# Optimization experiments

Hardware: AMD Instinct MI355X
Metric: run time of the kernel (lower is better)

The kernel has to match this reference:

```python
import jax, jax.numpy as jnp
import numpy as np

N = 50000      # num_nodes
E = 400000     # num_edges
ND = 128       # node_dim (== hidden_dim of GraphNetwork)
HID = 128      # per-head hidden dim in GAT layer
HEADS = 4      # GAT default num_heads
L = 3          # num_layers


def setup_inputs() -> dict:
    key = jax.random.key(0)
    ks = jax.random.split(key, 12)
    s = lambda k, shape, fan: (jax.random.normal(k, shape, jnp.float32) / np.sqrt(fan)).astype(jnp.float32)
    return dict(
        node_features=jax.random.normal(ks[0], (N, ND), jnp.float32),
        edge_index=jax.random.randint(ks[1], (2, E), 0, N, dtype=jnp.int32),
        enc_w1=s(ks[2], (ND, HID), ND), enc_b1=jnp.zeros((HID,), jnp.float32),
        enc_w2=s(ks[3], (HID, HID), HID), enc_b2=jnp.zeros((HID,), jnp.float32),
        gat_W=s(ks[4], (L, HID, HEADS * HID), HID),
        gat_a_src=s(ks[5], (L, HEADS, HID), HID),
        gat_a_dst=s(ks[6], (L, HEADS, HID), HID),
        gat_out_w=s(ks[7], (L, HEADS * HID, HID), HEADS * HID),
        gat_out_b=jnp.zeros((L, HID), jnp.float32),
        out_w1=s(ks[8], (HID, HID), HID), out_b1=jnp.zeros((HID,), jnp.float32),
        out_w2=s(ks[9], (HID, HID), HID), out_b2=jnp.zeros((HID,), jnp.float32),
    )


def _gat_layer(x, row, col, W, a_src, a_dst, ow, ob):
    """One GraphAttentionLayer (eval mode: dropout disabled)."""
    n = x.shape[0]
    h = (x @ W).reshape(n, HEADS, HID)                       # [N,H,D]
    # per-node attention logits (equivalent to (h[row]*a_src).sum(-1) gathered)
    s_src = jnp.einsum('nhd,hd->nh', h, a_src)               # [N,H]
    s_dst = jnp.einsum('nhd,hd->nh', h, a_dst)               # [N,H]
    e = s_src[row] + s_dst[col]                              # [E,H]
    e = jnp.where(e > 0, e, 0.2 * e)                         # LeakyReLU(0.2)
    e_exp = jnp.exp(e)                                       # matches torch: raw exp, no max-shift
    e_sum = jax.ops.segment_sum(e_exp, col, num_segments=n)  # [N,H]
    alpha = e_exp / (e_sum[col] + 1e-8)                      # [E,H]
    msg = h[row] * alpha[:, :, None]                         # [E,H,D]
    out = jax.ops.segment_sum(msg, col, num_segments=n)      # [N,H,D]
    out = out.reshape(n, HEADS * HID) @ ow + ob              # out_proj
    return x + out                                           # residual


def reference(node_features, edge_index, enc_w1, enc_b1, enc_w2, enc_b2,
              gat_W, gat_a_src, gat_a_dst, gat_out_w, gat_out_b,
              out_w1, out_b1, out_w2, out_b2):
    row, col = edge_index[0], edge_index[1]
    # node encoder: Linear-ReLU-Linear
    h = jax.nn.relu(node_features @ enc_w1 + enc_b1) @ enc_w2 + enc_b2
    for i in range(L):
        h = _gat_layer(h, row, col, gat_W[i], gat_a_src[i], gat_a_dst[i],
                       gat_out_w[i], gat_out_b[i])
    # output MLP: Linear-ReLU-Linear
    h = jax.nn.relu(h @ out_w1 + out_b1) @ out_w2 + out_b2
    # batch is None, global_pooling='mean'
    graph_embedding = h.mean(axis=0, keepdims=True)          # [1,HID]
    return h, graph_embedding
```

## Files before the change

### kernel.cpp

```cpp
#include <hip/hip_runtime.h>
#include <math.h>

typedef unsigned short ushort_t;
typedef __attribute__((ext_vector_type(8))) unsigned short ushortx8;
typedef __attribute__((ext_vector_type(4))) unsigned short ushortx4;
typedef __attribute__((ext_vector_type(4))) float floatx4;
typedef __attribute__((ext_vector_type(8))) short frag8;

__device__ __forceinline__ float bf2f(ushort_t u){
  union {unsigned int i; float f;} v; v.i = ((unsigned int)u)<<16; return v.f;
}
__device__ __forceinline__ ushort_t f2bf(float f){
  union {float f; unsigned int i;} v; v.f = f;
  unsigned int x = v.i;
  unsigned int r = x + 0x7fffu + ((x>>16)&1u);
  return (ushort_t)(r>>16);
}

__device__ __forceinline__ void gload16(const void* g, void* l){
  __builtin_amdgcn_global_load_lds(
      (const __attribute__((address_space(1))) unsigned int*)g,
      (__attribute__((address_space(3))) unsigned int*)l, 16, 0, 0);
}

__global__ __launch_bounds__(256) void k_count(const int* __restrict__ col, int* __restrict__ cnt, int E){
  int e = blockIdx.x*256 + threadIdx.x;
  if (e < E) atomicAdd(&cnt[col[e]], 1);
}

__global__ __launch_bounds__(256) void k_scan1(const int* __restrict__ cnt, int* __restrict__ offs,
                                               int* __restrict__ partials, int n){
  __shared__ int buf[256];
  int tid = threadIdx.x;
  int gid = blockIdx.x*256 + tid;
  int v = (gid < n) ? cnt[gid] : 0;
  buf[tid] = v; __syncthreads();
  #pragma unroll
  for (int off=1; off<256; off<<=1){
    int t = (tid >= off) ? buf[tid-off] : 0;
    __syncthreads();
    buf[tid] += t;
    __syncthreads();
  }
  if (gid < n) offs[gid] = buf[tid] - v;
  if (tid == 255) partials[blockIdx.x] = buf[255];
}

__global__ __launch_bounds__(256) void k_scan2(int* __restrict__ partials, int nb){
  __shared__ int buf[256];
  int tid = threadIdx.x;
  int v = (tid < nb) ? partials[tid] : 0;
  buf[tid] = v; __syncthreads();
  #pragma unroll
  for (int off=1; off<256; off<<=1){
    int t = (tid >= off) ? buf[tid-off] : 0;
    __syncthreads();
    buf[tid] += t;
    __syncthreads();
  }
  partials[tid] = buf[tid] - v;
}

__global__ __launch_bounds__(256) void k_scan3(int* __restrict__ offs, const int* __restrict__ partials,
                                               int n, int E){
  int gid = blockIdx.x*256 + threadIdx.x;
  if (gid < n) offs[gid] += partials[blockIdx.x];
  if (blockIdx.x == 0 && threadIdx.x == 0) offs[n] = E;
}

__global__ __launch_bounds__(256) void k_fill(const int* __restrict__ row, const int* __restrict__ col,
                                              const int* __restrict__ offs, int* __restrict__ fill,
                                              int* __restrict__ rowS, int E){
  int e = blockIdx.x*256 + threadIdx.x;
  if (e >= E) return;
  int c = col[e];
  int pos = offs[c] + atomicAdd(&fill[c], 1);
  rowS[pos] = row[e];
}

template<int K, int NC, int CNT>
__global__ __launch_bounds__(256) void k_convT_b(const float* __restrict__ src, ushort_t* __restrict__ dst){
  int idx = blockIdx.x*256 + threadIdx.x;
  if (idx >= CNT*K*NC) return;
  int l = idx / (K*NC);
  int rem = idx - l*(K*NC);
  int k = rem / NC, n = rem - k*NC;
  dst[(size_t)l*K*NC + (size_t)n*K + k] = f2bf(src[idx]);
}

__global__ __launch_bounds__(256) void k_convT4(const float* __restrict__ s0, const float* __restrict__ s1,
                                                const float* __restrict__ s2, const float* __restrict__ s3,
                                                ushort_t* __restrict__ d0, ushort_t* __restrict__ d1,
                                                ushort_t* __restrict__ d2, ushort_t* __restrict__ d3){
  int idx = blockIdx.x*256 + threadIdx.x;
  if (idx >= 4*16384) return;
  int which = idx >> 14;
  int rem = idx & 16383;
  int k = rem >> 7, n = rem & 127;
  const float* s = which==0 ? s0 : which==1 ? s1 : which==2 ? s2 : s3;
  ushort_t*    d = which==0 ? d0 : which==1 ? d1 : which==2 ? d2 : d3;
  d[n*128 + k] = f2bf(s[rem]);
}


__device__ __forceinline__ void stage_tile64(const ushort_t* src, int ld, int row0, int M, int kc,
                                             ushort_t* lds, int tid){
  int wid = tid>>6, lane = tid&63;
  #pragma unroll
  for (int i=0;i<4;i++){
    int chunk = wid*256 + i*64 + lane;
    int r = chunk>>3, c8 = chunk&7;
    int gr = row0 + r; if (gr >= M) gr = M-1;
    gload16(src + (size_t)gr*ld + kc + c8*8, (char*)lds + (size_t)chunk*16);
  }
}
__device__ __forceinline__ void stage_w128(const ushort_t* src, ushort_t* lds, int tid){
  #pragma unroll
  for (int i=0;i<8;i++){
    int chunk = tid + 256*i;
    gload16(src + (size_t)chunk*8, (char*)lds + (size_t)chunk*16);
  }
}

template<int SA,int SB,int NKS>
__device__ __forceinline__ void ldsgemm(const ushort_t* LA, const ushort_t* LB,
                                        floatx4 (&acc)[4][4], int wr,int wc,int lm,int lk){
  #pragma unroll
  for (int ks=0; ks<NKS; ks++){
    frag8 a[4], b[4];
    #pragma unroll
    for (int mi=0;mi<4;mi++) a[mi] = *(const frag8*)&LA[(wr+mi*16+lm)*SA + ks*32 + lk];
    #pragma unroll
    for (int ni=0;ni<4;ni++) b[ni] = *(const frag8*)&LB[(wc+ni*16+lm)*SB + ks*32 + lk];
    #pragma unroll
    for (int mi=0;mi<4;mi++)
      #pragma unroll
      for (int ni=0;ni<4;ni++)
        acc[mi][ni] = __builtin_amdgcn_mfma_f32_16x16x32_bf16(b[ni], a[mi], acc[mi][ni], 0, 0, 0);
  }
}

__device__ __forceinline__ void zero_acc(floatx4 (&acc)[4][4]){
  #pragma unroll
  for (int i=0;i<4;i++)
    #pragma unroll
    for (int j=0;j<4;j++) acc[i][j] = floatx4{0.f,0.f,0.f,0.f};
}

__device__ __forceinline__ void sdst_block(const floatx4 (&acc)[4][4],
    const float* avec_s, const float* avec_d, float* s_src, float* s_dst, float* sred,
    int head, int bm, int M, int tid, int wid, int lane, int wr, int wc, int lm, int lr4){
  floatx4 avs[4], avd[4];
  #pragma unroll
  for (int ni=0;ni<4;ni++){
    avs[ni] = *(const floatx4*)&avec_s[head*128 + wc + ni*16 + lr4];
    avd[ni] = *(const floatx4*)&avec_d[head*128 + wc + ni*16 + lr4];
  }
  #pragma unroll
  for (int mi=0;mi<4;mi++){
    float vs = 0.f, vd = 0.f;
    #pragma unroll
    for (int ni=0;ni<4;ni++)
      #pragma unroll
      for (int r=0;r<4;r++){
        float v = acc[mi][ni][r];
        vs += v * avs[ni][r];
        vd += v * avd[ni][r];
      }
    vs += __shfl_xor(vs, 16); vs += __shfl_xor(vs, 32);
    vd += __shfl_xor(vd, 16); vd += __shfl_xor(vd, 32);
    if (lane < 16){
      int rl = wr + mi*16 + lm;
      sred[0*256 + (wid&1)*128 + rl] = vs;
      sred[1*256 + (wid&1)*128 + rl] = vd;
    }
  }
  __syncthreads();
  int sd = tid >> 7, rl = tid & 127;
  float v = sred[sd*256 + rl] + sred[sd*256 + 128 + rl];
  int rowg = bm + rl;
  if (rowg < M) (sd ? s_dst : s_src)[(size_t)rowg*4 + head] = v;
}

__device__ __forceinline__ void wgemm_heads(const ushort_t* LA_xb, ushort_t* LB,
    const ushort_t* WT, const float* avs, const float* avd,
    ushort_t* h, float* s_src, float* s_dst, float* sred,
    int bm, int M, int tid, int wid, int lane, int wr, int wc, int lm, int lk, int lr4){
  for (int hb=0; hb<4; hb++){
    __syncthreads();
    stage_w128(WT + (size_t)hb*16384, LB, tid);
    __syncthreads();
    floatx4 acc[4][4]; zero_acc(acc);
    ldsgemm<128,128,4>(LA_xb, LB, acc, wr, wc, lm, lk);
    #pragma unroll
    for (int mi=0;mi<4;mi++){
      int rowg = bm + wr + mi*16 + lm;
      if (rowg < M){
        #pragma unroll
        for (int ni=0;ni<4;ni++){
          int coll = wc + ni*16 + lr4;
          ushortx4 o;
          #pragma unroll
          for (int r=0;r<4;r++) o[r] = f2bf(acc[mi][ni][r]);
          *(ushortx4*)&h[(size_t)rowg*512 + hb*128 + coll] = o;
        }
      }
    }
    sdst_block(acc, avs, avd, s_src, s_dst, sred, hb, bm, M, tid, wid, lane, wr, wc, lm, lr4);
  }
}

__global__ __launch_bounds__(256) void k_enc(
    const float* __restrict__ nodef,
    const ushort_t* __restrict__ e1T, const float* __restrict__ eb1,
    const ushort_t* __restrict__ e2T, const float* __restrict__ eb2,
    const ushort_t* __restrict__ WT, const float* __restrict__ avs, const float* __restrict__ avd,
    float* __restrict__ x, ushort_t* __restrict__ h,
    float* __restrict__ s_src, float* __restrict__ s_dst, int M)
{
  __shared__ ushort_t LA[128*128];
  __shared__ ushort_t LB[128*128];
  __shared__ float sred[512];
  const int tid = threadIdx.x, wid = tid>>6, lane = tid&63;
  const int bm = blockIdx.x*128;
  const int wr = (wid>>1)*64, wc = (wid&1)*64, lm = lane&15, lk = (lane>>4)*8, lr4 = (lane>>4)*4;

  #pragma unroll
  for (int i=0;i<8;i++){
    int chunk = tid + 256*i;
    int r = chunk>>4, c8 = chunk&15;
    int gr = bm + r; if (gr >= M) gr = M-1;
    floatx4 lo = *(const floatx4*)(nodef + (size_t)gr*128 + c8*8);
    floatx4 hi = *(const floatx4*)(nodef + (size_t)gr*128 + c8*8 + 4);
    ushortx8 v;
    #pragma unroll
    for (int j=0;j<4;j++){ v[j] = f2bf(lo[j]); v[j+4] = f2bf(hi[j]); }
    *(ushortx8*)&LA[r*128 + c8*8] = v;
  }
  stage_w128(e1T, LB, tid);
  __syncthreads();

  floatx4 acc[4][4]; zero_acc(acc);
  ldsgemm<128,128,4>(LA, LB, acc, wr, wc, lm, lk);
  __syncthreads();
  #pragma unroll
  for (int mi=0;mi<4;mi++){
    int rl = wr + mi*16 + lm;
    #pragma unroll
    for (int ni=0;ni<4;ni++){
      int coll = wc + ni*16 + lr4;
      floatx4 b4 = *(const floatx4*)&eb1[coll];
      ushortx4 o;
      #pragma unroll
      for (int r=0;r<4;r++){
        float v = acc[mi][ni][r] + b4[r];
        v = v > 0.f ? v : 0.f;
        o[r] = f2bf(v);
      }
      *(ushortx4*)&LA[rl*128 + coll] = o;
    }
  }
  stage_w128(e2T, LB, tid);
  __syncthreads();

  zero_acc(acc);
  ldsgemm<128,128,4>(LA, LB, acc, wr, wc, lm, lk);
  __syncthreads();
  #pragma unroll
  for (int mi=0;mi<4;mi++){
    int rl = wr + mi*16 + lm;
    int rowg = bm + rl;
    #pragma unroll
    for (int ni=0;ni<4;ni++){
      int coll = wc + ni*16 + lr4;
      floatx4 b4 = *(const floatx4*)&eb2[coll];
      floatx4 v;
      #pragma unroll
      for (int r=0;r<4;r++) v[r] = acc[mi][ni][r] + b4[r];
      if (rowg < M) *(floatx4*)&x[(size_t)rowg*128 + coll] = v;
      ushortx4 o;
      #pragma unroll
      for (int r=0;r<4;r++) o[r] = f2bf(v[r]);
      *(ushortx4*)&LA[rl*128 + coll] = o;
    }
  }

  wgemm_heads(LA, LB, WT, avs, avd, h, s_src, s_dst, sred,
              bm, M, tid, wid, lane, wr, wc, lm, lk, lr4);
}

__global__ __launch_bounds__(256) void k_mid(
    const ushort_t* __restrict__ msg, const ushort_t* __restrict__ OT, const float* __restrict__ ob,
    const ushort_t* __restrict__ WT, const float* __restrict__ avs, const float* __restrict__ avd,
    float* __restrict__ x, ushort_t* __restrict__ h,
    float* __restrict__ s_src, float* __restrict__ s_dst, int M)
{
  __shared__ ushort_t LA[128*128];
  __shared__ ushort_t LB[128*128];
  __shared__ float sred[512];
  const int tid = threadIdx.x, wid = tid>>6, lane = tid&63;
  const int bm = blockIdx.x*128;
  const int wr = (wid>>1)*64, wc = (wid&1)*64, lm = lane&15, lk = (lane>>4)*8, lr4 = (lane>>4)*4;

  floatx4 acc[4][4]; zero_acc(acc);
  for (int kc = 0; kc < 512; kc += 64){
    stage_tile64(msg, 512, bm, M, kc, LA, tid);
    stage_tile64(OT,  512, 0, 128, kc, LB, tid);
    __syncthreads();
    ldsgemm<64,64,2>(LA, LB, acc, wr, wc, lm, lk);
    __syncthreads();
  }
  #pragma unroll
  for (int mi=0;mi<4;mi++){
    int rl = wr + mi*16 + lm;
    int rowg = bm + rl;
    #pragma unroll
    for (int ni=0;ni<4;ni++){
      int coll = wc + ni*16 + lr4;
      floatx4 b4 = *(const floatx4*)&ob[coll];
      floatx4 v;
      #pragma unroll
      for (int r=0;r<4;r++) v[r] = acc[mi][ni][r] + b4[r];
      if (rowg < M){
        floatx4 xo = *(const floatx4*)&x[(size_t)rowg*128 + coll];
        #pragma unroll
        for (int r=0;r<4;r++) v[r] += xo[r];
        *(floatx4*)&x[(size_t)rowg*128 + coll] = v;
      }
      ushortx4 o;
      #pragma unroll
      for (int r=0;r<4;r++) o[r] = f2bf(v[r]);
      *(ushortx4*)&LA[rl*128 + coll] = o;
    }
  }

  wgemm_heads(LA, LB, WT, avs, avd, h, s_src, s_dst, sred,
              bm, M, tid, wid, lane, wr, wc, lm, lk, lr4);
}

__global__ __launch_bounds__(256) void k_tail(
    const ushort_t* __restrict__ msg, const ushort_t* __restrict__ OT, const float* __restrict__ ob,
    const ushort_t* __restrict__ m1T, const float* __restrict__ mb1,
    const ushort_t* __restrict__ m2T, const float* __restrict__ mb2,
    const float* __restrict__ x, float* __restrict__ out, float* __restrict__ cpart, int M)
{
  __shared__ ushort_t LA[128*128];
  __shared__ ushort_t LB[128*128];
  __shared__ float sredc[256];
  const int tid = threadIdx.x, wid = tid>>6, lane = tid&63;
  const int bm = blockIdx.x*128;
  const int wr = (wid>>1)*64, wc = (wid&1)*64, lm = lane&15, lk = (lane>>4)*8, lr4 = (lane>>4)*4;

  floatx4 acc[4][4]; zero_acc(acc);
  for (int kc = 0; kc < 512; kc += 64){
    stage_tile64(msg, 512, bm, M, kc, LA, tid);
    stage_tile64(OT,  512, 0, 128, kc, LB, tid);
    __syncthreads();
    ldsgemm<64,64,2>(LA, LB, acc, wr, wc, lm, lk);
    __syncthreads();
  }
  #pragma unroll
  for (int mi=0;mi<4;mi++){
    int rl = wr + mi*16 + lm;
    int rowg = bm + rl;
    #pragma unroll
    for (int ni=0;ni<4;ni++){
      int coll = wc + ni*16 + lr4;
      floatx4 b4 = *(const floatx4*)&ob[coll];
      floatx4 v;
      #pragma unroll
      for (int r=0;r<4;r++) v[r] = acc[mi][ni][r] + b4[r];
      if (rowg < M){
        floatx4 xo = *(const floatx4*)&x[(size_t)rowg*128 + coll];
        #pragma unroll
        for (int r=0;r<4;r++) v[r] += xo[r];
      }
      ushortx4 o;
      #pragma unroll
      for (int r=0;r<4;r++) o[r] = f2bf(v[r]);
      *(ushortx4*)&LA[rl*128 + coll] = o;
    }
  }
  stage_w128(m1T, LB, tid);
  __syncthreads();

  zero_acc(acc);
  ldsgemm<128,128,4>(LA, LB, acc, wr, wc, lm, lk);
  __syncthreads();
  #pragma unroll
  for (int mi=0;mi<4;mi++){
    int rl = wr + mi*16 + lm;
    #pragma unroll
    for (int ni=0;ni<4;ni++){
      int coll = wc + ni*16 + lr4;
      floatx4 b4 = *(const floatx4*)&mb1[coll];
      ushortx4 o;
      #pragma unroll
      for (int r=0;r<4;r++){
        float v = acc[mi][ni][r] + b4[r];
        v = v > 0.f ? v : 0.f;
        o[r] = f2bf(v);
      }
      *(ushortx4*)&LA[rl*128 + coll] = o;
    }
  }
  stage_w128(m2T, LB, tid);
  __syncthreads();

  zero_acc(acc);
  ldsgemm<128,128,4>(LA, LB, acc, wr, wc, lm, lk);

  float csum[4][4];
  #pragma unroll
  for (int i=0;i<4;i++)
    #pragma unroll
    for (int r=0;r<4;r++) csum[i][r] = 0.f;
  #pragma unroll
  for (int mi=0;mi<4;mi++){
    int rowg = bm + wr + mi*16 + lm;
    #pragma unroll
    for (int ni=0;ni<4;ni++){
      int coll = wc + ni*16 + lr4;
      floatx4 b4 = *(const floatx4*)&mb2[coll];
      floatx4 v;
      #pragma unroll
      for (int r=0;r<4;r++) v[r] = acc[mi][ni][r] + b4[r];
      if (rowg < M){
        *(floatx4*)&out[(size_t)rowg*128 + coll] = v;
        #pragma unroll
        for (int r=0;r<4;r++) csum[ni][r] += v[r];
      }
    }
  }
  __syncthreads();
  #pragma unroll
  for (int ni=0;ni<4;ni++)
    #pragma unroll
    for (int r=0;r<4;r++){
      float cs = csum[ni][r];
      cs += __shfl_xor(cs, 1);
      cs += __shfl_xor(cs, 2);
      cs += __shfl_xor(cs, 4);
      cs += __shfl_xor(cs, 8);
      if (lm == 0) sredc[(wid>>1)*128 + wc + ni*16 + lr4 + r] = cs;
    }
  __syncthreads();
  if (tid < 128) cpart[(size_t)blockIdx.x*128 + tid] = sredc[tid] + sredc[128 + tid];
}

__global__ __launch_bounds__(256) void k_gather(const ushort_t* __restrict__ h,
    const float* __restrict__ s_src, const float* __restrict__ s_dst,
    const int* __restrict__ offs, const int* __restrict__ rowS,
    ushort_t* __restrict__ msg, int N)
{
  int wid = threadIdx.x >> 6, lane = threadIdx.x & 63;
  int n = blockIdx.x*4 + wid;
  if (n >= N) return;
  int beg = offs[n], end = offs[n+1];
  const int sub  = lane & 15;
  const int head = lane >> 4;
  const float sdv = s_dst[(size_t)n*4 + head];
  const int c0 = lane*8;

  float acc[8];
  #pragma unroll
  for (int k=0;k<8;k++) acc[k] = 0.f;
  float dsum = 0.f;

  for (int chunk = beg; chunk < end; chunk += 16){
    int m = end - chunk; if (m > 16) m = 16;
    int q = chunk + (sub < m ? sub : m-1);
    int r_p = rowS[q];
    float ss = s_src[(size_t)r_p*4 + head];
    float e = ss + sdv;
    e = e > 0.f ? e : 0.2f*e;
    float w = __expf(e);
    if (sub >= m) w = 0.f;
    dsum += w;

    int j = 0;
    for (; j+1 < m; j += 2){
      int r0 = __shfl(r_p, j);
      int r1 = __shfl(r_p, j+1);
      float w0 = __shfl(w, head*16 + j);
      float w1 = __shfl(w, head*16 + j+1);
      ushortx8 h0 = *(const ushortx8*)(h + (size_t)r0*512 + c0);
      ushortx8 h1 = *(const ushortx8*)(h + (size_t)r1*512 + c0);
      #pragma unroll
      for (int k=0;k<8;k++) acc[k] += w0 * bf2f(h0[k]);
      #pragma unroll
      for (int k=0;k<8;k++) acc[k] += w1 * bf2f(h1[k]);
    }
    if (j < m){
      int r0 = __shfl(r_p, j);
      float w0 = __shfl(w, head*16 + j);
      ushortx8 h0 = *(const ushortx8*)(h + (size_t)r0*512 + c0);
      #pragma unroll
      for (int k=0;k<8;k++) acc[k] += w0 * bf2f(h0[k]);
    }
  }

  float d = dsum;
  #pragma unroll
  for (int mask=1; mask<16; mask<<=1) d += __shfl_xor(d, mask);
  float invd = 1.0f / (d + 1e-8f);

  ushortx8 o;
  #pragma unroll
  for (int k=0;k<8;k++) o[k] = f2bf(acc[k]*invd);
  __builtin_nontemporal_store(o, (ushortx8*)(msg + (size_t)n*512 + c0));
}

__global__ __launch_bounds__(256) void k_csum2(const float* __restrict__ part, float* __restrict__ out,
                                               int nb, int N){
  __shared__ float buf[256];
  int c = threadIdx.x & 127, half = threadIdx.x >> 7;
  float s = 0.f;
  for (int b = half; b < nb; b += 2) s += part[(size_t)b*128 + c];
  buf[threadIdx.x] = s; __syncthreads();
  if (threadIdx.x < 128) out[c] = (buf[c] + buf[128 + c]) / (float)N;
}

extern "C" void kernel_launch(void* const* d_in, const int* in_sizes, int n_in,
                              void* d_out, int out_size, void* d_ws, size_t ws_size,
                              hipStream_t stream)
{
  const int N = in_sizes[0] / 128;
  const int E = in_sizes[1] / 2;

  const float* nodef  = (const float*)d_in[0];
  const int*   row    = (const int*)d_in[1];
  const int*   col    = row + E;
  const float* enc_w1 = (const float*)d_in[2];
  const float* enc_b1 = (const float*)d_in[3];
  const float* enc_w2 = (const float*)d_in[4];
  const float* enc_b2 = (const float*)d_in[5];
  const float* gat_W  = (const float*)d_in[6];
  const float* a_src  = (const float*)d_in[7];
  const float* a_dst  = (const float*)d_in[8];
  const float* out_w  = (const float*)d_in[9];
  const float* out_b  = (const float*)d_in[10];
  const float* w1     = (const float*)d_in[11];
  const float* b1     = (const float*)d_in[12];
  const float* w2     = (const float*)d_in[13];
  const float* b2     = (const float*)d_in[14];

  char* p = (char*)d_ws;
  auto alloc = [&](size_t bytes)->char*{
    char* r = p; p += (bytes + 255) & ~(size_t)255; return r;
  };
  float*    x     = (float*)   alloc((size_t)N*128*4);
  ushort_t* msg   = (ushort_t*)alloc((size_t)N*512*2);
  ushort_t* h     = (ushort_t*)alloc((size_t)N*512*2);
  float*    s_src = (float*)   alloc((size_t)N*4*4);
  float*    s_dst = (float*)   alloc((size_t)N*4*4);
  int*      offs  = (int*)     alloc(((size_t)N+1)*4);
  int*      rowS  = (int*)     alloc((size_t)E*4);
  int*      cnt   = (int*)     alloc((size_t)N*4);
  int*      fill  = (int*)     alloc((size_t)N*4);
  int*      parts = (int*)     alloc(1024);
  float*    cpart = (float*)   alloc((size_t)((N+127)/128)*128*4);
  ushort_t* wt_e1 = (ushort_t*)alloc(16384*2);
  ushort_t* wt_e2 = (ushort_t*)alloc(16384*2);
  ushort_t* wt_W  = (ushort_t*)alloc((size_t)3*65536*2);
  ushort_t* wt_o  = (ushort_t*)alloc((size_t)3*65536*2);
  ushort_t* wt_m1 = (ushort_t*)alloc(16384*2);
  ushort_t* wt_m2 = (ushort_t*)alloc(16384*2);

  hipMemsetAsync(cnt, 0, (size_t)N*4, stream);
  hipMemsetAsync(fill, 0, (size_t)N*4, stream);

  const int gE = (E + 255)/256;
  const int gN = (N + 255)/256;
  const int gW = (N + 3)/4;
  const int gy = (N + 127)/128;
  dim3 blk(256);

  k_count<<<gE, blk, 0, stream>>>(col, cnt, E);
  k_scan1<<<gN, blk, 0, stream>>>(cnt, offs, parts, N);
  k_scan2<<<1,  blk, 0, stream>>>(parts, gN);
  k_scan3<<<gN, blk, 0, stream>>>(offs, parts, N, E);
  k_fill <<<gE, blk, 0, stream>>>(row, col, offs, fill, rowS, E);

  k_convT4<<<(4*16384+255)/256, blk, 0, stream>>>(enc_w1, enc_w2, w1, w2, wt_e1, wt_e2, wt_m1, wt_m2);
  k_convT_b<128,512,3><<<(3*65536+255)/256, blk, 0, stream>>>(gat_W, wt_W);
  k_convT_b<512,128,3><<<(3*65536+255)/256, blk, 0, stream>>>(out_w, wt_o);

  k_enc<<<gy, blk, 0, stream>>>(nodef, wt_e1, enc_b1, wt_e2, enc_b2,
                                wt_W, a_src, a_dst, x, h, s_src, s_dst, N);

  for (int l = 0; l < 3; l++){
    k_gather<<<gW, blk, 0, stream>>>(h, s_src, s_dst, offs, rowS, msg, N);
    if (l < 2){
      k_mid<<<gy, blk, 0, stream>>>(msg, wt_o + (size_t)l*65536, out_b + (size_t)l*128,
                                    wt_W + (size_t)(l+1)*65536,
                                    a_src + (size_t)(l+1)*512, a_dst + (size_t)(l+1)*512,
                                    x, h, s_src, s_dst, N);
    } else {
      k_tail<<<gy, blk, 0, stream>>>(msg, wt_o + (size_t)2*65536, out_b + (size_t)2*128,
                                     wt_m1, b1, wt_m2, b2,
                                     x, (float*)d_out, cpart, N);
    }
  }
  k_csum2<<<1, blk, 0, stream>>>(cpart, (float*)d_out + (size_t)N*128, gy, N);
}
```

Measured before the change: 511.0 us.

## Double-buffer weight and activation LDS staging across all fused GEMM kernels

Replaces the single-buffered LDS staging (load tile, sync, compute, sync) with a two-slot ping-pong scheme. The next 64-wide K slice of weights and messages is issued via global_load_lds while the current slice feeds the MFMAs. Weight tiles are also prefetched during epilogues. The aim is to hide global-load latency behind compute. The cost is more complex buffer indexing and synchronisation, with the same LDS footprint.

```diff
diff --git a/kernel.cpp b/kernel.cpp
--- a/kernel.cpp
+++ b/kernel.cpp
@@ -114,13 +114,6 @@
     gload16(src + (size_t)gr*ld + kc + c8*8, (char*)lds + (size_t)chunk*16);
   }
 }
-__device__ __forceinline__ void stage_w128(const ushort_t* src, ushort_t* lds, int tid){
-  #pragma unroll
-  for (int i=0;i<8;i++){
-    int chunk = tid + 256*i;
-    gload16(src + (size_t)chunk*8, (char*)lds + (size_t)chunk*16);
-  }
-}
 
 template<int SA,int SB,int NKS>
 __device__ __forceinline__ void ldsgemm(const ushort_t* LA, const ushort_t* LB,
@@ -182,31 +175,39 @@
   if (rowg < M) (sd ? s_dst : s_src)[(size_t)rowg*4 + head] = v;
 }
 
-__device__ __forceinline__ void wgemm_heads(const ushort_t* LA_xb, ushort_t* LB,
-    const ushort_t* WT, const float* avs, const float* avd,
-    ushort_t* h, float* s_src, float* s_dst, float* sred,
+__device__ __forceinline__ void wgemm_heads_db(ushort_t* SM,
+    const ushort_t* __restrict__ WT, const float* avsv, const float* avdv,
+    ushort_t* __restrict__ h, float* __restrict__ s_src, float* __restrict__ s_dst, float* sred,
     int bm, int M, int tid, int wid, int lane, int wr, int wc, int lm, int lk, int lr4){
-  for (int hb=0; hb<4; hb++){
-    __syncthreads();
-    stage_w128(WT + (size_t)hb*16384, LB, tid);
-    __syncthreads();
-    floatx4 acc[4][4]; zero_acc(acc);
-    ldsgemm<128,128,4>(LA_xb, LB, acc, wr, wc, lm, lk);
-    #pragma unroll
-    for (int mi=0;mi<4;mi++){
-      int rowg = bm + wr + mi*16 + lm;
-      if (rowg < M){
-        #pragma unroll
-        for (int ni=0;ni<4;ni++){
-          int coll = wc + ni*16 + lr4;
-          ushortx4 o;
+  floatx4 acc[4][4];
+  #pragma unroll
+  for (int ht=0; ht<8; ht++){
+    const int cur = ht&1;
+    if (ht<7){
+      const int nhb = (ht+1)>>1, nkph = (ht+1)&1;
+      stage_tile64(WT + (size_t)nhb*16384, 128, 0, 128, nkph*64, SM + 16384 + (cur^1)*8192, tid);
+    }
+    if ((ht&1)==0) zero_acc(acc);
+    ldsgemm<128,64,2>(SM + (ht&1)*64, SM + 16384 + cur*8192, acc, wr, wc, lm, lk);
+    if (ht&1){
+      const int hb = ht>>1;
+      #pragma unroll
+      for (int mi=0;mi<4;mi++){
+        int rowg = bm + wr + mi*16 + lm;
+        if (rowg < M){
           #pragma unroll
-          for (int r=0;r<4;r++) o[r] = f2bf(acc[mi][ni][r]);
-          *(ushortx4*)&h[(size_t)rowg*512 + hb*128 + coll] = o;
+          for (int ni=0;ni<4;ni++){
+            int coll = wc + ni*16 + lr4;
+            ushortx4 o;
+            #pragma unroll
+            for (int r=0;r<4;r++) o[r] = f2bf(acc[mi][ni][r]);
+            *(ushortx4*)&h[(size_t)rowg*512 + hb*128 + coll] = o;
+          }
         }
       }
-    }
-    sdst_block(acc, avs, avd, s_src, s_dst, sred, hb, bm, M, tid, wid, lane, wr, wc, lm, lr4);
+      sdst_block(acc, avsv, avdv, s_src, s_dst, sred, hb, bm, M, tid, wid, lane, wr, wc, lm, lr4);
+    }
+    __syncthreads();
   }
 }
 
@@ -218,12 +219,13 @@
     float* __restrict__ x, ushort_t* __restrict__ h,
     float* __restrict__ s_src, float* __restrict__ s_dst, int M)
 {
-  __shared__ ushort_t LA[128*128];
-  __shared__ ushort_t LB[128*128];
+  __shared__ ushort_t SM[32768];
   __shared__ float sred[512];
   const int tid = threadIdx.x, wid = tid>>6, lane = tid&63;
   const int bm = blockIdx.x*128;
   const int wr = (wid>>1)*64, wc = (wid&1)*64, lm = lane&15, lk = (lane>>4)*8, lr4 = (lane>>4)*4;
+  ushort_t* SB0 = SM + 16384;
+  ushort_t* SB1 = SM + 24576;
 
   #pragma unroll
   for (int i=0;i<8;i++){
@@ -235,14 +237,20 @@
     ushortx8 v;
     #pragma unroll
     for (int j=0;j<4;j++){ v[j] = f2bf(lo[j]); v[j+4] = f2bf(hi[j]); }
-    *(ushortx8*)&LA[r*128 + c8*8] = v;
-  }
-  stage_w128(e1T, LB, tid);
+    *(ushortx8*)&SM[r*128 + c8*8] = v;
+  }
+  stage_tile64(e1T, 128, 0, 128, 0, SB0, tid);
   __syncthreads();
 
   floatx4 acc[4][4]; zero_acc(acc);
-  ldsgemm<128,128,4>(LA, LB, acc, wr, wc, lm, lk);
-  __syncthreads();
+  stage_tile64(e1T, 128, 0, 128, 64, SB1, tid);
+  ldsgemm<128,64,2>(SM + 0, SB0, acc, wr, wc, lm, lk);
+  __syncthreads();
+  stage_tile64(e2T, 128, 0, 128, 0, SB0, tid);
+  ldsgemm<128,64,2>(SM + 64, SB1, acc, wr, wc, lm, lk);
+  __syncthreads();
+
+  stage_tile64(e2T, 128, 0, 128, 64, SB1, tid);
   #pragma unroll
   for (int mi=0;mi<4;mi++){
     int rl = wr + mi*16 + lm;
@@ -257,15 +265,18 @@
         v = v > 0.f ? v : 0.f;
         o[r] = f2bf(v);
       }
-      *(ushortx4*)&LA[rl*128 + coll] = o;
-    }
-  }
-  stage_w128(e2T, LB, tid);
+      *(ushortx4*)&SM[rl*128 + coll] = o;
+    }
+  }
   __syncthreads();
 
   zero_acc(acc);
-  ldsgemm<128,128,4>(LA, LB, acc, wr, wc, lm, lk);
-  __syncthreads();
+  ldsgemm<128,64,2>(SM + 0, SB0, acc, wr, wc, lm, lk);
+  __syncthreads();
+  stage_tile64(WT, 128, 0, 128, 0, SB0, tid);
+  ldsgemm<128,64,2>(SM + 64, SB1, acc, wr, wc, lm, lk);
+  __syncthreads();
+
   #pragma unroll
   for (int mi=0;mi<4;mi++){
     int rl = wr + mi*16 + lm;
@@ -281,12 +292,13 @@
       ushortx4 o;
       #pragma unroll
       for (int r=0;r<4;r++) o[r] = f2bf(v[r]);
-      *(ushortx4*)&LA[rl*128 + coll] = o;
-    }
-  }
-
-  wgemm_heads(LA, LB, WT, avs, avd, h, s_src, s_dst, sred,
-              bm, M, tid, wid, lane, wr, wc, lm, lk, lr4);
+      *(ushortx4*)&SM[rl*128 + coll] = o;
+    }
+  }
+  __syncthreads();
+
+  wgemm_heads_db(SM, WT, avs, avd, h, s_src, s_dst, sred,
+                 bm, M, tid, wid, lane, wr, wc, lm, lk, lr4);
 }
 
 __global__ __launch_bounds__(256) void k_mid(
@@ -295,21 +307,28 @@
     float* __restrict__ x, ushort_t* __restrict__ h,
     float* __restrict__ s_src, float* __restrict__ s_dst, int M)
 {
-  __shared__ ushort_t LA[128*128];
-  __shared__ ushort_t LB[128*128];
+  __shared__ ushort_t SM[32768];
   __shared__ float sred[512];
   const int tid = threadIdx.x, wid = tid>>6, lane = tid&63;
   const int bm = blockIdx.x*128;
   const int wr = (wid>>1)*64, wc = (wid&1)*64, lm = lane&15, lk = (lane>>4)*8, lr4 = (lane>>4)*4;
 
   floatx4 acc[4][4]; zero_acc(acc);
-  for (int kc = 0; kc < 512; kc += 64){
-    stage_tile64(msg, 512, bm, M, kc, LA, tid);
-    stage_tile64(OT,  512, 0, 128, kc, LB, tid);
+  stage_tile64(msg, 512, bm, M, 0, SM, tid);
+  stage_tile64(OT,  512, 0, 128, 0, SM + 16384, tid);
+  __syncthreads();
+  #pragma unroll
+  for (int t=0; t<8; t++){
+    const int cur = t&1;
+    if (t<7){
+      stage_tile64(msg, 512, bm, M, (t+1)*64, SM + (cur^1)*8192, tid);
+      stage_tile64(OT,  512, 0, 128, (t+1)*64, SM + 16384 + (cur^1)*8192, tid);
+    }
+    ldsgemm<64,64,2>(SM + cur*8192, SM + 16384 + cur*8192, acc, wr, wc, lm, lk);
     __syncthreads();
-    ldsgemm<64,64,2>(LA, LB, acc, wr, wc, lm, lk);
-    __syncthreads();
-  }
+  }
+
+  stage_tile64(WT, 128, 0, 128, 0, SM + 16384, tid);
   #pragma unroll
   for (int mi=0;mi<4;mi++){
     int rl = wr + mi*16 + lm;
@@ -330,12 +349,13 @@
       ushortx4 o;
       #pragma unroll
       for (int r=0;r<4;r++) o[r] = f2bf(v[r]);
-      *(ushortx4*)&LA[rl*128 + coll] = o;
-    }
-  }
-
-  wgemm_heads(LA, LB, WT, avs, avd, h, s_src, s_dst, sred,
-              bm, M, tid, wid, lane, wr, wc, lm, lk, lr4);
+      *(ushortx4*)&SM[rl*128 + coll] = o;
+    }
+  }
+  __syncthreads();
+
+  wgemm_heads_db(SM, WT, avs, avd, h, s_src, s_dst, sred,
+                 bm, M, tid, wid, lane, wr, wc, lm, lk, lr4);
 }
 
 __global__ __launch_bounds__(256) void k_tail(
@@ -344,21 +364,30 @@
     const ushort_t* __restrict__ m2T, const float* __restrict__ mb2,
     const float* __restrict__ x, float* __restrict__ out, float* __restrict__ cpart, int M)
 {
-  __shared__ ushort_t LA[128*128];
-  __shared__ ushort_t LB[128*128];
+  __shared__ ushort_t SM[32768];
   __shared__ float sredc[256];
   const int tid = threadIdx.x, wid = tid>>6, lane = tid&63;
   const int bm = blockIdx.x*128;
   const int wr = (wid>>1)*64, wc = (wid&1)*64, lm = lane&15, lk = (lane>>4)*8, lr4 = (lane>>4)*4;
+  ushort_t* SB0 = SM + 16384;
+  ushort_t* SB1 = SM + 24576;
 
   floatx4 acc[4][4]; zero_acc(acc);
-  for (int kc = 0; kc < 512; kc += 64){
-    stage_tile64(msg, 512, bm, M, kc, LA, tid);
-    stage_tile64(OT,  512, 0, 128, kc, LB, tid);
+  stage_tile64(msg, 512, bm, M, 0, SM, tid);
+  stage_tile64(OT,  512, 0, 128, 0, SB0, tid);
+  __syncthreads();
+  #pragma unroll
+  for (int t=0; t<8; t++){
+    const int cur = t&1;
+    if (t<7){
+      stage_tile64(msg, 512, bm, M, (t+1)*64, SM + (cur^1)*8192, tid);
+      stage_tile64(OT,  512, 0, 128, (t+1)*64, SM + 16384 + (cur^1)*8192, tid);
+    }
+    ldsgemm<64,64,2>(SM + cur*8192, SM + 16384 + cur*8192, acc, wr, wc, lm, lk);
     __syncthreads();
-    ldsgemm<64,64,2>(LA, LB, acc, wr, wc, lm, lk);
-    __syncthreads();
-  }
+  }
+
+  stage_tile64(m1T, 128, 0, 128, 0, SB0, tid);
   #pragma unroll
   for (int mi=0;mi<4;mi++){
     int rl = wr + mi*16 + lm;
@@ -378,15 +407,20 @@
       ushortx4 o;
       #pragma unroll
       for (int r=0;r<4;r++) o[r] = f2bf(v[r]);
-      *(ushortx4*)&LA[rl*128 + coll] = o;
-    }
-  }
-  stage_w128(m1T, LB, tid);
+      *(ushortx4*)&SM[rl*128 + coll] = o;
+    }
+  }
   __syncthreads();
 
   zero_acc(acc);
-  ldsgemm<128,128,4>(LA, LB, acc, wr, wc, lm, lk);
-  __syncthreads();
+  stage_tile64(m1T, 128, 0, 128, 64, SB1, tid);
+  ldsgemm<128,64,2>(SM + 0, SB0, acc, wr, wc, lm, lk);
+  __syncthreads();
+  stage_tile64(m2T, 128, 0, 128, 0, SB0, tid);
+  ldsgemm<128,64,2>(SM + 64, SB1, acc, wr, wc, lm, lk);
+  __syncthreads();
+
+  stage_tile64(m2T, 128, 0, 128, 64, SB1, tid);
   #pragma unroll
   for (int mi=0;mi<4;mi++){
     int rl = wr + mi*16 + lm;
@@ -401,14 +435,15 @@
         v = v > 0.f ? v : 0.f;
         o[r] = f2bf(v);
       }
-      *(ushortx4*)&LA[rl*128 + coll] = o;
-    }
-  }
-  stage_w128(m2T, LB, tid);
+      *(ushortx4*)&SM[rl*128 + coll] = o;
+    }
+  }
   __syncthreads();
 
   zero_acc(acc);
-  ldsgemm<128,128,4>(LA, LB, acc, wr, wc, lm, lk);
+  ldsgemm<128,64,2>(SM + 0, SB0, acc, wr, wc, lm, lk);
+  __syncthreads();
+  ldsgemm<128,64,2>(SM + 64, SB1, acc, wr, wc, lm, lk);
 
   float csum[4][4];
   #pragma unroll
```

Result: no change. 512.4 us (+0.3%).
